# Performance work log

Measured on AMD Instinct MI355X. Metric: run time of the kernel, lower is better.

## Reference

```python
import jax, jax.numpy as jnp
import numpy as np

B, S, F, H, L = 4096, 512, 8, 10, 2


def setup_inputs() -> dict:
    key = jax.random.key(0)
    ks = jax.random.split(key, 12)
    bound = 1.0 / np.sqrt(H)  # PyTorch LSTM/Linear init scale
    u = lambda k, shape: jax.random.uniform(k, shape, jnp.float32, -bound, bound)
    return {
        "input_tensor": jax.random.normal(ks[0], (B, S, F), jnp.float32),
        "hidden": jnp.zeros((L, B, H), jnp.float32),
        "cell": jnp.zeros((L, B, H), jnp.float32),
        # layer 0 (input size F), layer 1 (input size H); gate order i,f,g,o
        "W_ih0": u(ks[1], (4 * H, F)), "W_hh0": u(ks[2], (4 * H, H)),
        "b_ih0": u(ks[3], (4 * H,)),   "b_hh0": u(ks[4], (4 * H,)),
        "W_ih1": u(ks[5], (4 * H, H)), "W_hh1": u(ks[6], (4 * H, H)),
        "b_ih1": u(ks[7], (4 * H,)),   "b_hh1": u(ks[8], (4 * H,)),
        "W_fc": u(ks[9], (1, H)),      "b_fc": u(ks[10], (1,)),
    }


def _lstm_layer(x_sbf, h0, c0, W_ih, W_hh, b_ih, b_hh):
    # x_sbf: [S, B, Fin]; h0,c0: [B, H]. Returns hs [S,B,H], (hT, cT).
    b = b_ih + b_hh

    def step(carry, x):
        h, c = carry
        gates = x @ W_ih.T + h @ W_hh.T + b  # [B, 4H]
        i, f, g, o = jnp.split(gates, 4, axis=-1)
        c = jax.nn.sigmoid(f) * c + jax.nn.sigmoid(i) * jnp.tanh(g)
        h = jax.nn.sigmoid(o) * jnp.tanh(c)
        return (h, c), h

    (hT, cT), hs = jax.lax.scan(step, (h0, c0), x_sbf)
    return hs, hT, cT


def reference(input_tensor, hidden, cell,
              W_ih0, W_hh0, b_ih0, b_hh0,
              W_ih1, W_hh1, b_ih1, b_hh1,
              W_fc, b_fc):
    x = jnp.transpose(input_tensor, (1, 0, 2))  # [S, B, F]
    hs0, h0T, c0T = _lstm_layer(x, hidden[0], cell[0], W_ih0, W_hh0, b_ih0, b_hh0)
    hs1, h1T, c1T = _lstm_layer(hs0, hidden[1], cell[1], W_ih1, W_hh1, b_ih1, b_hh1)
    out = hs1[-1]                      # last timestep, [B, H]
    out_regression = out @ W_fc.T + b_fc  # [B, 1]
    hidden_out = jnp.stack([h0T, h1T])
    cell_out = jnp.stack([c0T, c1T])
    return out_regression, hidden_out, cell_out
```

## Files before the change

### kernel.cpp

```cpp
#include <hip/hip_runtime.h>


typedef __fp16 v2h __attribute__((ext_vector_type(2)));
typedef __fp16 v8h __attribute__((ext_vector_type(8)));
struct h4 { v2h a, b, c, d; };

#define L2E 1.4426950408889634f

__device__ __forceinline__ v2h pkh(float a, float b) {
    return __builtin_amdgcn_cvt_pkrtz(a, b);
}

#define SIGM(a)  __builtin_amdgcn_rcpf(1.0f + __builtin_amdgcn_exp2f(-(a)))
#define TANHP(a) fmaf(-2.0f, __builtin_amdgcn_rcpf(1.0f + __builtin_amdgcn_exp2f(a)), 1.0f)
#define DOT2(acc, w, v) (acc) = __builtin_amdgcn_fdot2((w), (v), (acc), false)

#define READROW(PTR, H)                                                      \
    { v8h w0_ = *(const v8h*)(PTR);                                          \
      v2h w1_ = *(const v2h*)((PTR) + 8);                                    \
      h4 q_ = __builtin_bit_cast(h4, w0_);                                   \
      H[0]=q_.a; H[1]=q_.b; H[2]=q_.c; H[3]=q_.d; H[4]=w1_; }

__global__ __launch_bounds__(128, 2)
void lstm2_r13(const float* __restrict__ x,
               const float* __restrict__ hid,
               const float* __restrict__ cel,
               const float* __restrict__ Wih0, const float* __restrict__ Whh0,
               const float* __restrict__ bih0, const float* __restrict__ bhh0,
               const float* __restrict__ Wih1, const float* __restrict__ Whh1,
               const float* __restrict__ bih1, const float* __restrict__ bhh1,
               const float* __restrict__ Wfc,  const float* __restrict__ bfc,
               float* __restrict__ out)
{
    __shared__ __attribute__((aligned(16))) __fp16 h0buf[16][6][16];
    __shared__ __attribute__((aligned(16))) __fp16 h1buf[6][16];
    __shared__ float fcb[6][10];

    const int tid  = threadIdx.x;
    const int lane = tid & 63;
    const int uwid = __builtin_amdgcn_readfirstlane(tid >> 6);
    int g = lane / 10;
    int j = lane - g * 10;
    if (lane >= 60) { g = 5; j = 9; }
    const bool live = (lane < 60);
    const int e  = blockIdx.x * 6 + g;
    const int ec = (e < 4095) ? e : 4095;
    const bool st = live && (e < 4096);

    if (uwid == 0) {
        v2h w[4][9]; float bb[4];
        #pragma unroll
        for (int q = 0; q < 4; ++q) {
            const int r = q * 10 + j;
            const float sc = (q == 2) ? 2.0f * L2E : L2E;
            #pragma unroll
            for (int k = 0; k < 4; ++k)
                w[q][k] = pkh(Wih0[r*8+2*k]*sc, Wih0[r*8+2*k+1]*sc);
            #pragma unroll
            for (int k = 0; k < 5; ++k)
                w[q][4+k] = pkh(Whh0[r*10+2*k]*sc, Whh0[r*10+2*k+1]*sc);
            bb[q] = (bih0[r] + bhh0[r]) * sc;
        }
        v2h hv[5];
        #pragma unroll
        for (int k = 0; k < 5; ++k) hv[k] = pkh(hid[ec*10+2*k], hid[ec*10+2*k+1]);
        float cc = cel[ec * 10 + j];
        float hj = 0.0f;

        __fp16* const wrow = &h0buf[0][g][0];

        const float4* __restrict__ xp4 = reinterpret_cast<const float4*>(x + (size_t)ec * 4096);
        float4 xa[2], xb[2], xc[2], xd[2];
        xa[0]=xp4[0]; xa[1]=xp4[1];  xb[0]=xp4[2]; xb[1]=xp4[3];
        xc[0]=xp4[4]; xc[1]=xp4[5];  xd[0]=xp4[6]; xd[1]=xp4[7];

#define L0STEP(S, XB, ROFF, DO_REF)                                          \
        {                                                                    \
            v2h x0=pkh(XB[0].x,XB[0].y), x1=pkh(XB[0].z,XB[0].w);            \
            v2h x2=pkh(XB[1].x,XB[1].y), x3=pkh(XB[1].z,XB[1].w);            \
            if (DO_REF) { XB[0]=xr[ROFF]; XB[1]=xr[(ROFF)+1]; }              \
            float aI=bb[0], aF=bb[1], aG=bb[2], aO=bb[3];                    \
            DOT2(aI,w[0][0],x0); DOT2(aF,w[1][0],x0);                        \
            DOT2(aG,w[2][0],x0); DOT2(aO,w[3][0],x0);                        \
            DOT2(aI,w[0][1],x1); DOT2(aF,w[1][1],x1);                        \
            DOT2(aG,w[2][1],x1); DOT2(aO,w[3][1],x1);                        \
            DOT2(aI,w[0][2],x2); DOT2(aF,w[1][2],x2);                        \
            DOT2(aG,w[2][2],x2); DOT2(aO,w[3][2],x2);                        \
            DOT2(aI,w[0][3],x3); DOT2(aF,w[1][3],x3);                        \
            DOT2(aG,w[2][3],x3); DOT2(aO,w[3][3],x3);                        \
            _Pragma("unroll")                                                \
            for (int k = 0; k < 5; ++k) {                                    \
                DOT2(aI,w[0][4+k],hv[k]); DOT2(aF,w[1][4+k],hv[k]);          \
                DOT2(aG,w[2][4+k],hv[k]); DOT2(aO,w[3][4+k],hv[k]);          \
            }                                                                \
            float i_=SIGM(aI), f_=SIGM(aF), g_=TANHP(aG), o_=SIGM(aO);       \
            cc = fmaf(f_, cc, i_ * g_);                                      \
            hj = o_ * TANHP((2.0f*L2E) * cc);                                \
            wrow[(S)*96 + j] = (__fp16)hj;                                   \
            READROW(wrow + (S)*96, hv)                                       \
        }

        for (int it = 0; it < 31; ++it) {
            const float4* __restrict__ xr = xp4 + 32 * it;
            L0STEP(0,  xa, 8,  1)  L0STEP(1,  xb, 10, 1)
            L0STEP(2,  xc, 12, 1)  L0STEP(3,  xd, 14, 1)
            L0STEP(4,  xa, 16, 1)  L0STEP(5,  xb, 18, 1)
            L0STEP(6,  xc, 20, 1)  L0STEP(7,  xd, 22, 1)
            __syncthreads();
            L0STEP(8,  xa, 24, 1)  L0STEP(9,  xb, 26, 1)
            L0STEP(10, xc, 28, 1)  L0STEP(11, xd, 30, 1)
            L0STEP(12, xa, 32, 1)  L0STEP(13, xb, 34, 1)
            L0STEP(14, xc, 36, 1)  L0STEP(15, xd, 38, 1)
            __syncthreads();
        }
        {
            const float4* __restrict__ xr = xp4 + 992;
            L0STEP(0,  xa, 8,  1)  L0STEP(1,  xb, 10, 1)
            L0STEP(2,  xc, 12, 1)  L0STEP(3,  xd, 14, 1)
            L0STEP(4,  xa, 16, 1)  L0STEP(5,  xb, 18, 1)
            L0STEP(6,  xc, 20, 1)  L0STEP(7,  xd, 22, 1)
            __syncthreads();
            L0STEP(8,  xa, 24, 1)  L0STEP(9,  xb, 26, 1)
            L0STEP(10, xc, 28, 1)  L0STEP(11, xd, 30, 1)
            L0STEP(12, xa, 0, 0)   L0STEP(13, xb, 0, 0)
            L0STEP(14, xc, 0, 0)   L0STEP(15, xd, 0, 0)
            __syncthreads();
        }
#undef L0STEP

        if (st) {
            out[4096          + e * 10 + j] = hj;
            out[4096 + 81920  + e * 10 + j] = cc;
        }

    } else {
        v2h w[4][10]; float bb[4];
        #pragma unroll
        for (int q = 0; q < 4; ++q) {
            const int r = q * 10 + j;
            const float sc = (q == 2) ? 2.0f * L2E : L2E;
            #pragma unroll
            for (int k = 0; k < 5; ++k) {
                w[q][k]   = pkh(Wih1[r*10+2*k]*sc, Wih1[r*10+2*k+1]*sc);
                w[q][5+k] = pkh(Whh1[r*10+2*k]*sc, Whh1[r*10+2*k+1]*sc);
            }
            bb[q] = (bih1[r] + bhh1[r]) * sc;
        }
        v2h hv[5];
        #pragma unroll
        for (int k = 0; k < 5; ++k) hv[k] = pkh(hid[40960+ec*10+2*k], hid[40960+ec*10+2*k+1]);
        float cc = cel[40960 + ec * 10 + j];
        float hj = 0.0f;

        const __fp16* const rbase = &h0buf[0][g][0];
        __fp16* const h1r = &h1buf[g][0];

#define L1STEP(S)                                                            \
        {                                                                    \
            v2h p[5];                                                        \
            READROW(rbase + (S)*96, p)                                       \
            float aI=bb[0], aF=bb[1], aG=bb[2], aO=bb[3];                    \
            _Pragma("unroll")                                                \
            for (int k = 0; k < 5; ++k) {                                    \
                DOT2(aI,w[0][5+k],hv[k]); DOT2(aF,w[1][5+k],hv[k]);          \
                DOT2(aG,w[2][5+k],hv[k]); DOT2(aO,w[3][5+k],hv[k]);          \
            }                                                                \
            _Pragma("unroll")                                                \
            for (int k = 0; k < 5; ++k) {                                    \
                DOT2(aI,w[0][k],p[k]); DOT2(aF,w[1][k],p[k]);                \
                DOT2(aG,w[2][k],p[k]); DOT2(aO,w[3][k],p[k]);                \
            }                                                                \
            float i_=SIGM(aI), f_=SIGM(aF), g_=TANHP(aG), o_=SIGM(aO);       \
            cc = fmaf(f_, cc, i_ * g_);                                      \
            hj = o_ * TANHP((2.0f*L2E) * cc);                                \
            h1r[j] = (__fp16)hj;                                             \
            READROW(h1r, hv)                                                 \
        }

        for (int it = 0; it < 32; ++it) {
            __syncthreads();
            L1STEP(0)  L1STEP(1)  L1STEP(2)  L1STEP(3)
            L1STEP(4)  L1STEP(5)  L1STEP(6)  L1STEP(7)
            __syncthreads();
            L1STEP(8)  L1STEP(9)  L1STEP(10) L1STEP(11)
            L1STEP(12) L1STEP(13) L1STEP(14) L1STEP(15)
        }
#undef L1STEP

        if (live) fcb[g][j] = hj * Wfc[j];
        if (st) {
            out[4096 + 40960  + e * 10 + j] = hj;
            out[4096 + 122880 + e * 10 + j] = cc;
        }
        if (st && j == 0) {
            float p = bfc[0];
            #pragma unroll
            for (int k = 0; k < 10; ++k) p += fcb[g][k];
            out[e] = p;
        }
    }
}

extern "C" void kernel_launch(void* const* d_in, const int* in_sizes, int n_in,
                              void* d_out, int out_size, void* d_ws, size_t ws_size,
                              hipStream_t stream) {
    const float* x    = (const float*)d_in[0];
    const float* hid  = (const float*)d_in[1];
    const float* cel  = (const float*)d_in[2];
    const float* Wih0 = (const float*)d_in[3];
    const float* Whh0 = (const float*)d_in[4];
    const float* bih0 = (const float*)d_in[5];
    const float* bhh0 = (const float*)d_in[6];
    const float* Wih1 = (const float*)d_in[7];
    const float* Whh1 = (const float*)d_in[8];
    const float* bih1 = (const float*)d_in[9];
    const float* bhh1 = (const float*)d_in[10];
    const float* Wfc  = (const float*)d_in[11];
    const float* bfc  = (const float*)d_in[12];

    hipLaunchKernelGGL(lstm2_r13, dim3(683), dim3(128), 0, stream,
                       x, hid, cel, Wih0, Whh0, bih0, bhh0,
                       Wih1, Whh1, bih1, bhh1, Wfc, bfc,
                       (float*)d_out);
}
```

Measured before the change: 170.3 us.

## Run both LSTM layers in one wavefront with a skewed per-step pipeline

Replaces the two-wavefront producer/consumer split, where wave 0 ran layer 0 and wave 1 ran layer 1 with block barriers every 8 steps, with a single 64-lane wavefront. Half the lane groups run layer 0 and the other half run layer 1, one timestep behind, passing hidden state through a 4-slot LDS ring. Because everything happens inside one wave, __syncthreads disappears and the inter-layer handoff follows wave lockstep order. Each block now covers 3 sequences instead of 6, so the grid doubles to 1366 blocks of 64 threads. Every lane executes the same padded 40-dot body, which adds select overhead and some wasted dot products for layer 0, and prologue/epilogue masking handles the one-step skew.

```diff
diff --git a/kernel.cpp b/kernel.cpp
--- a/kernel.cpp
+++ b/kernel.cpp
@@ -21,8 +21,8 @@
       h4 q_ = __builtin_bit_cast(h4, w0_);                                   \
       H[0]=q_.a; H[1]=q_.b; H[2]=q_.c; H[3]=q_.d; H[4]=w1_; }
 
-__global__ __launch_bounds__(128, 2)
-void lstm2_r13(const float* __restrict__ x,
+__global__ __launch_bounds__(64, 2)
+void lstm2_r14(const float* __restrict__ x,
                const float* __restrict__ hid,
                const float* __restrict__ cel,
                const float* __restrict__ Wih0, const float* __restrict__ Whh0,
@@ -32,162 +32,134 @@
                const float* __restrict__ Wfc,  const float* __restrict__ bfc,
                float* __restrict__ out)
 {
-    __shared__ __attribute__((aligned(16))) __fp16 h0buf[16][6][16];
-    __shared__ __attribute__((aligned(16))) __fp16 h1buf[6][16];
-    __shared__ float fcb[6][10];
+    __shared__ __attribute__((aligned(16))) __fp16 h0s[4][3][16];
+    __shared__ __attribute__((aligned(16))) __fp16 h1w[3][16];
+    __shared__ float fcb[3][10];
 
-    const int tid  = threadIdx.x;
-    const int lane = tid & 63;
-    const int uwid = __builtin_amdgcn_readfirstlane(tid >> 6);
-    int g = lane / 10;
-    int j = lane - g * 10;
+    const int lane = threadIdx.x & 63;
+    int g = lane / 10, j = lane - (lane / 10) * 10;
     if (lane >= 60) { g = 5; j = 9; }
-    const bool live = (lane < 60);
-    const int e  = blockIdx.x * 6 + g;
-    const int ec = (e < 4095) ? e : 4095;
-    const bool st = live && (e < 4096);
+    const bool role = (g >= 3);
+    const int  ge   = role ? g - 3 : g;
+    const int  e    = blockIdx.x * 3 + ge;
+    const int  ec   = (e < 4095) ? e : 4095;
+    const bool st   = (lane < 60) && (e < 4096);
 
-    if (uwid == 0) {
-        v2h w[4][9]; float bb[4];
-        #pragma unroll
-        for (int q = 0; q < 4; ++q) {
-            const int r = q * 10 + j;
-            const float sc = (q == 2) ? 2.0f * L2E : L2E;
-            #pragma unroll
-            for (int k = 0; k < 4; ++k)
-                w[q][k] = pkh(Wih0[r*8+2*k]*sc, Wih0[r*8+2*k+1]*sc);
-            #pragma unroll
-            for (int k = 0; k < 5; ++k)
-                w[q][4+k] = pkh(Whh0[r*10+2*k]*sc, Whh0[r*10+2*k+1]*sc);
-            bb[q] = (bih0[r] + bhh0[r]) * sc;
-        }
-        v2h hv[5];
-        #pragma unroll
-        for (int k = 0; k < 5; ++k) hv[k] = pkh(hid[ec*10+2*k], hid[ec*10+2*k+1]);
-        float cc = cel[ec * 10 + j];
-        float hj = 0.0f;
-
-        __fp16* const wrow = &h0buf[0][g][0];
-
-        const float4* __restrict__ xp4 = reinterpret_cast<const float4*>(x + (size_t)ec * 4096);
-        float4 xa[2], xb[2], xc[2], xd[2];
-        xa[0]=xp4[0]; xa[1]=xp4[1];  xb[0]=xp4[2]; xb[1]=xp4[3];
-        xc[0]=xp4[4]; xc[1]=xp4[5];  xd[0]=xp4[6]; xd[1]=xp4[7];
-
-#define L0STEP(S, XB, ROFF, DO_REF)                                          \
-        {                                                                    \
-            v2h x0=pkh(XB[0].x,XB[0].y), x1=pkh(XB[0].z,XB[0].w);            \
-            v2h x2=pkh(XB[1].x,XB[1].y), x3=pkh(XB[1].z,XB[1].w);            \
-            if (DO_REF) { XB[0]=xr[ROFF]; XB[1]=xr[(ROFF)+1]; }              \
-            float aI=bb[0], aF=bb[1], aG=bb[2], aO=bb[3];                    \
-            DOT2(aI,w[0][0],x0); DOT2(aF,w[1][0],x0);                        \
-            DOT2(aG,w[2][0],x0); DOT2(aO,w[3][0],x0);                        \
-            DOT2(aI,w[0][1],x1); DOT2(aF,w[1][1],x1);                        \
-            DOT2(aG,w[2][1],x1); DOT2(aO,w[3][1],x1);                        \
-            DOT2(aI,w[0][2],x2); DOT2(aF,w[1][2],x2);                        \
-            DOT2(aG,w[2][2],x2); DOT2(aO,w[3][2],x2);                        \
-            DOT2(aI,w[0][3],x3); DOT2(aF,w[1][3],x3);                        \
-            DOT2(aG,w[2][3],x3); DOT2(aO,w[3][3],x3);                        \
-            _Pragma("unroll")                                                \
-            for (int k = 0; k < 5; ++k) {                                    \
-                DOT2(aI,w[0][4+k],hv[k]); DOT2(aF,w[1][4+k],hv[k]);          \
-                DOT2(aG,w[2][4+k],hv[k]); DOT2(aO,w[3][4+k],hv[k]);          \
-            }                                                                \
-            float i_=SIGM(aI), f_=SIGM(aF), g_=TANHP(aG), o_=SIGM(aO);       \
-            cc = fmaf(f_, cc, i_ * g_);                                      \
-            hj = o_ * TANHP((2.0f*L2E) * cc);                                \
-            wrow[(S)*96 + j] = (__fp16)hj;                                   \
-            READROW(wrow + (S)*96, hv)                                       \
-        }
-
-        for (int it = 0; it < 31; ++it) {
-            const float4* __restrict__ xr = xp4 + 32 * it;
-            L0STEP(0,  xa, 8,  1)  L0STEP(1,  xb, 10, 1)
-            L0STEP(2,  xc, 12, 1)  L0STEP(3,  xd, 14, 1)
-            L0STEP(4,  xa, 16, 1)  L0STEP(5,  xb, 18, 1)
-            L0STEP(6,  xc, 20, 1)  L0STEP(7,  xd, 22, 1)
-            __syncthreads();
-            L0STEP(8,  xa, 24, 1)  L0STEP(9,  xb, 26, 1)
-            L0STEP(10, xc, 28, 1)  L0STEP(11, xd, 30, 1)
-            L0STEP(12, xa, 32, 1)  L0STEP(13, xb, 34, 1)
-            L0STEP(14, xc, 36, 1)  L0STEP(15, xd, 38, 1)
-            __syncthreads();
-        }
-        {
-            const float4* __restrict__ xr = xp4 + 992;
-            L0STEP(0,  xa, 8,  1)  L0STEP(1,  xb, 10, 1)
-            L0STEP(2,  xc, 12, 1)  L0STEP(3,  xd, 14, 1)
-            L0STEP(4,  xa, 16, 1)  L0STEP(5,  xb, 18, 1)
-            L0STEP(6,  xc, 20, 1)  L0STEP(7,  xd, 22, 1)
-            __syncthreads();
-            L0STEP(8,  xa, 24, 1)  L0STEP(9,  xb, 26, 1)
-            L0STEP(10, xc, 28, 1)  L0STEP(11, xd, 30, 1)
-            L0STEP(12, xa, 0, 0)   L0STEP(13, xb, 0, 0)
-            L0STEP(14, xc, 0, 0)   L0STEP(15, xd, 0, 0)
-            __syncthreads();
-        }
-#undef L0STEP
-
-        if (st) {
-            out[4096          + e * 10 + j] = hj;
-            out[4096 + 81920  + e * 10 + j] = cc;
-        }
-
-    } else {
-        v2h w[4][10]; float bb[4];
-        #pragma unroll
-        for (int q = 0; q < 4; ++q) {
-            const int r = q * 10 + j;
-            const float sc = (q == 2) ? 2.0f * L2E : L2E;
+    v2h w[4][10]; float bb[4];
+    #pragma unroll
+    for (int q = 0; q < 4; ++q) {
+        const int r = q * 10 + j;
+        const float sc = (q == 2) ? 2.0f * L2E : L2E;
+        if (role) {
             #pragma unroll
             for (int k = 0; k < 5; ++k) {
                 w[q][k]   = pkh(Wih1[r*10+2*k]*sc, Wih1[r*10+2*k+1]*sc);
                 w[q][5+k] = pkh(Whh1[r*10+2*k]*sc, Whh1[r*10+2*k+1]*sc);
             }
             bb[q] = (bih1[r] + bhh1[r]) * sc;
+        } else {
+            #pragma unroll
+            for (int k = 0; k < 4; ++k)
+                w[q][k] = pkh(Wih0[r*8+2*k]*sc, Wih0[r*8+2*k+1]*sc);
+            w[q][4] = pkh(0.0f, 0.0f);
+            #pragma unroll
+            for (int k = 0; k < 5; ++k)
+                w[q][5+k] = pkh(Whh0[r*10+2*k]*sc, Whh0[r*10+2*k+1]*sc);
+            bb[q] = (bih0[r] + bhh0[r]) * sc;
         }
-        v2h hv[5];
-        #pragma unroll
-        for (int k = 0; k < 5; ++k) hv[k] = pkh(hid[40960+ec*10+2*k], hid[40960+ec*10+2*k+1]);
-        float cc = cel[40960 + ec * 10 + j];
-        float hj = 0.0f;
+    }
+    const float wfc = Wfc[j];
 
-        const __fp16* const rbase = &h0buf[0][g][0];
-        __fp16* const h1r = &h1buf[g][0];
+    const float* hb = hid + (role ? 40960 : 0);
+    const float* cb = cel + (role ? 40960 : 0);
+    v2h hv[5];
+    #pragma unroll
+    for (int k = 0; k < 5; ++k) hv[k] = pkh(hb[ec*10+2*k], hb[ec*10+2*k+1]);
+    float cc = cb[ec*10 + j];
+    float hj = hb[ec*10 + j];
 
-#define L1STEP(S)                                                            \
-        {                                                                    \
-            v2h p[5];                                                        \
-            READROW(rbase + (S)*96, p)                                       \
-            float aI=bb[0], aF=bb[1], aG=bb[2], aO=bb[3];                    \
-            _Pragma("unroll")                                                \
-            for (int k = 0; k < 5; ++k) {                                    \
-                DOT2(aI,w[0][5+k],hv[k]); DOT2(aF,w[1][5+k],hv[k]);          \
-                DOT2(aG,w[2][5+k],hv[k]); DOT2(aO,w[3][5+k],hv[k]);          \
-            }                                                                \
-            _Pragma("unroll")                                                \
-            for (int k = 0; k < 5; ++k) {                                    \
-                DOT2(aI,w[0][k],p[k]); DOT2(aF,w[1][k],p[k]);                \
-                DOT2(aG,w[2][k],p[k]); DOT2(aO,w[3][k],p[k]);                \
-            }                                                                \
-            float i_=SIGM(aI), f_=SIGM(aF), g_=TANHP(aG), o_=SIGM(aO);       \
-            cc = fmaf(f_, cc, i_ * g_);                                      \
-            hj = o_ * TANHP((2.0f*L2E) * cc);                                \
-            h1r[j] = (__fp16)hj;                                             \
-            READROW(h1r, hv)                                                 \
+    __fp16* wrj[4]; const __fp16* rb[4]; const __fp16* ain[4];
+    #pragma unroll
+    for (int p = 0; p < 4; ++p) {
+        __fp16* own = role ? &h1w[ge][0] : &h0s[p][ge][0];
+        wrj[p] = own + j;
+        rb[p]  = own;
+        ain[p] = &h0s[p][ge][0];
+    }
+    if (role) h1w[ge][j] = (__fp16)hj;
+
+    const float4* __restrict__ xp4 = reinterpret_cast<const float4*>(x + (size_t)ec * 4096);
+    float4 xa[2], xb[2], xc[2], xd[2];
+    xa[0]=xp4[0]; xa[1]=xp4[1];  xb[0]=xp4[2]; xb[1]=xp4[3];
+    xc[0]=xp4[4]; xc[1]=xp4[5];  xd[0]=xp4[6]; xd[1]=xp4[7];
+
+    v2h sl[5], xin[5];
+    #pragma unroll
+    for (int k = 0; k < 5; ++k) sl[k] = pkh(0.0f, 0.0f);
+    xin[0]=pkh(xa[0].x,xa[0].y); xin[1]=pkh(xa[0].z,xa[0].w);
+    xin[2]=pkh(xa[1].x,xa[1].y); xin[3]=pkh(xa[1].z,xa[1].w);
+    xin[4]=pkh(0.0f,0.0f);
+
+#define BODY(XBN, XBR, P, PIN, TN, SUP, DOREF)                               \
+    {                                                                        \
+        v2h in0 = role ? sl[0] : xin[0];                                     \
+        v2h in1 = role ? sl[1] : xin[1];                                     \
+        v2h in2 = role ? sl[2] : xin[2];                                     \
+        v2h in3 = role ? sl[3] : xin[3];                                     \
+        v2h in4 = sl[4];                            \
+        float aI=bb[0], aF=bb[1], aG=bb[2], aO=bb[3];                        \
+        DOT2(aI,w[0][0],in0); DOT2(aF,w[1][0],in0);                          \
+        DOT2(aG,w[2][0],in0); DOT2(aO,w[3][0],in0);                          \
+        DOT2(aI,w[0][1],in1); DOT2(aF,w[1][1],in1);                          \
+        DOT2(aG,w[2][1],in1); DOT2(aO,w[3][1],in1);                          \
+        DOT2(aI,w[0][2],in2); DOT2(aF,w[1][2],in2);                          \
+        DOT2(aG,w[2][2],in2); DOT2(aO,w[3][2],in2);                          \
+        DOT2(aI,w[0][3],in3); DOT2(aF,w[1][3],in3);                          \
+        DOT2(aG,w[2][3],in3); DOT2(aO,w[3][3],in3);                          \
+        DOT2(aI,w[0][4],in4); DOT2(aF,w[1][4],in4);                          \
+        DOT2(aG,w[2][4],in4); DOT2(aO,w[3][4],in4);                          \
+        _Pragma("unroll")                                                    \
+        for (int k = 0; k < 5; ++k) {                                        \
+            DOT2(aI,w[0][5+k],hv[k]); DOT2(aF,w[1][5+k],hv[k]);              \
+            DOT2(aG,w[2][5+k],hv[k]); DOT2(aO,w[3][5+k],hv[k]);              \
+        }                                                                    \
+        float i_=SIGM(aI), f_=SIGM(aF), g_=TANHP(aG), o_=SIGM(aO);           \
+        float ncc = fmaf(f_, cc, i_ * g_);                                   \
+        float nhj = o_ * TANHP((2.0f*L2E) * ncc);                            \
+        if (SUP == 1) { ncc = role ? cc : ncc; nhj = role ? hj : nhj; }      \
+        if (SUP == 2) { ncc = role ? ncc : cc; nhj = role ? nhj : hj; }      \
+        cc = ncc; hj = nhj;                                                  \
+        *wrj[P] = (__fp16)hj;                                                \
+        READROW(rb[P], hv)                                                   \
+        READROW(ain[PIN], sl)                                                \
+        xin[0]=pkh(XBN[0].x,XBN[0].y); xin[1]=pkh(XBN[0].z,XBN[0].w);        \
+        xin[2]=pkh(XBN[1].x,XBN[1].y); xin[3]=pkh(XBN[1].z,XBN[1].w);        \
+        if (DOREF) { int tn=(TN)>511?511:(TN);                               \
+                     XBR[0]=xp4[2*tn]; XBR[1]=xp4[2*tn+1]; }                 \
+    }
+
+    BODY(xb, xa, 0, 3, 4, 1, 1)
+    BODY(xc, xb, 1, 0, 5, 1, 1)
+    for (int it = 0; it < 127; ++it) {
+        const int tb = 4 * it;
+        BODY(xd, xc, 2, 1, tb + 6, 0, 1)
+        BODY(xa, xd, 3, 2, tb + 7, 0, 1)
+        BODY(xb, xa, 0, 3, tb + 8, 0, 1)
+        BODY(xc, xb, 1, 0, tb + 9, 0, 1)
+    }
+    BODY(xd, xc, 2, 1, 511, 0, 0)
+    BODY(xa, xd, 3, 2, 511, 0, 0)
+    BODY(xb, xa, 0, 3, 511, 2, 0)
+    BODY(xc, xb, 1, 0, 511, 2, 0)
+#undef BODY
+
+    if (!role) {
+        if (st) {
+            out[4096          + e * 10 + j] = hj;
+            out[4096 + 81920  + e * 10 + j] = cc;
         }
-
-        for (int it = 0; it < 32; ++it) {
-            __syncthreads();
-            L1STEP(0)  L1STEP(1)  L1STEP(2)  L1STEP(3)
-            L1STEP(4)  L1STEP(5)  L1STEP(6)  L1STEP(7)
-            __syncthreads();
-            L1STEP(8)  L1STEP(9)  L1STEP(10) L1STEP(11)
-            L1STEP(12) L1STEP(13) L1STEP(14) L1STEP(15)
-        }
-#undef L1STEP
-
-        if (live) fcb[g][j] = hj * Wfc[j];
+    } else {
+        fcb[ge][j] = hj * wfc;
         if (st) {
             out[4096 + 40960  + e * 10 + j] = hj;
             out[4096 + 122880 + e * 10 + j] = cc;
@@ -195,7 +167,7 @@
         if (st && j == 0) {
             float p = bfc[0];
             #pragma unroll
-            for (int k = 0; k < 10; ++k) p += fcb[g][k];
+            for (int k = 0; k < 10; ++k) p += fcb[ge][k];
             out[e] = p;
         }
     }
@@ -218,7 +190,7 @@
     const float* Wfc  = (const float*)d_in[11];
     const float* bfc  = (const float*)d_in[12];
 
-    hipLaunchKernelGGL(lstm2_r13, dim3(683), dim3(128), 0, stream,
+    hipLaunchKernelGGL(lstm2_r14, dim3(1366), dim3(64), 0, stream,
                        x, hid, cel, Wih0, Whh0, bih0, bhh0,
                        Wih1, Whh1, bih1, bhh1, Wfc, bfc,
                        (float*)d_out);
```

Result: slower. 184.3 us (+8.2%).
